# Optimization experiments

Measured on AMD Instinct MI355X. Metric: run time of the kernel, lower is better.

## Reference

```python
import jax, jax.numpy as jnp
import numpy as np

B, T, H = 2, 2048, 512
E, K, INTER = 8, 2, 1024


def setup_inputs() -> dict:
    key = jax.random.key(0)
    ks = jax.random.split(key, 8)
    s_h = 1.0 / np.sqrt(H)
    s_i = 1.0 / np.sqrt(INTER)
    return {
        "x": jax.random.normal(ks[0], (B, T, H), dtype=jnp.float32),
        "router_w": jax.random.normal(ks[1], (H, E), dtype=jnp.float32) * s_h,
        "Wg": jax.random.normal(ks[2], (E, H, INTER), dtype=jnp.float32) * s_h,
        "Wu": jax.random.normal(ks[3], (E, H, INTER), dtype=jnp.float32) * s_h,
        "Wd": jax.random.normal(ks[4], (E, INTER, H), dtype=jnp.float32) * s_i,
        "Sg": jax.random.normal(ks[5], (H, INTER), dtype=jnp.float32) * s_h,
        "Su": jax.random.normal(ks[6], (H, INTER), dtype=jnp.float32) * s_h,
        "Sd": jax.random.normal(ks[7], (INTER, H), dtype=jnp.float32) * s_i,
    }


def reference(x, router_w, Wg, Wu, Wd, Sg, Su, Sd):
    b, t, h = x.shape
    flat = x.reshape(b * t, h)                        # [N, H]
    n = flat.shape[0]

    # --- router: softmax over experts, top-k, renormalized top-k weights ---
    full_scores = jax.nn.softmax(flat @ router_w, axis=-1)   # [N, E]
    w, idx = jax.lax.top_k(full_scores, K)                   # [N, K]
    w = w / jnp.sum(w, axis=-1, keepdims=True)

    # dense combine-weight matrix: cw[n, e] = sum_j w[n, j] * (idx[n, j] == e)
    cw = jnp.zeros((n, E), dtype=flat.dtype).at[jnp.arange(n)[:, None], idx].add(w)

    # --- routed experts (SwiGLU), computed for all experts, combined by cw ---
    g = jnp.einsum("nh,ehi->eni", flat, Wg)          # [E, N, INTER]
    u = jnp.einsum("nh,ehi->eni", flat, Wu)
    y = jnp.einsum("eni,eih->enh", jax.nn.silu(g) * u, Wd)   # [E, N, H]
    out = jnp.einsum("ne,enh->nh", cw, y)            # [N, H]

    # --- shared expert(s) ---
    out = out + (jax.nn.silu(flat @ Sg) * (flat @ Su)) @ Sd

    return out.reshape(b, t, h)
```

## Files before the change

### kernel.cpp

```cpp
#include <hip/hip_runtime.h>

typedef unsigned short u16;
typedef u16 u16x8 __attribute__((ext_vector_type(8)));
typedef __bf16 bf16x8 __attribute__((ext_vector_type(8)));
typedef float f32x4 __attribute__((ext_vector_type(4)));

constexpr int NT   = 4096;
constexpr int HD   = 512;
constexpr int ID   = 1024;
constexpr int NEXP = 8;
constexpr int ROWCAP = 13312;
constexpr int MAXRB  = 104;

constexpr size_t OFF_XB   = 0;
constexpr size_t OFF_WGT  = OFF_XB   + (size_t)NT*HD*2;
constexpr size_t OFF_WUT  = OFF_WGT  + (size_t)NEXP*ID*HD*2;
constexpr size_t OFF_WDT  = OFF_WUT  + (size_t)NEXP*ID*HD*2;
constexpr size_t OFF_SGT  = OFF_WDT  + (size_t)NEXP*HD*ID*2;
constexpr size_t OFF_SUT  = OFF_SGT  + (size_t)ID*HD*2;
constexpr size_t OFF_SDT  = OFF_SUT  + (size_t)ID*HD*2;
constexpr size_t OFF_HBUF = OFF_SDT  + (size_t)HD*ID*2;
constexpr size_t OFF_TOK  = OFF_HBUF + (size_t)ROWCAP*ID*2;
constexpr size_t OFF_WGTW = OFF_TOK  + (size_t)ROWCAP*4;
constexpr size_t OFF_TI   = OFF_WGTW + (size_t)ROWCAP*4;
constexpr size_t OFF_TW   = OFF_TI   + (size_t)NT*16;
constexpr size_t OFF_META = OFF_TW   + (size_t)NT*8;
constexpr size_t WS_NEED  = OFF_META + 2048;

__device__ __forceinline__ u16 f2bf(float f){
  unsigned int u = __float_as_uint(f);
  u += 0x7fffu + ((u >> 16) & 1u);
  return (u16)(u >> 16);
}

#define AS1C(p) ((const __attribute__((address_space(1))) void*)(p))
#define AS3(p)  ((__attribute__((address_space(3))) void*)(p))
__device__ __forceinline__ void gld16(const void* g, void* l){
  __builtin_amdgcn_global_load_lds(AS1C(g), AS3(l), 16, 0, 0);
}

__global__ __launch_bounds__(256) void transpose_convert_kernel(
    const float* __restrict__ Wg, const float* __restrict__ Wu, const float* __restrict__ Wd,
    const float* __restrict__ Sg, const float* __restrict__ Su, const float* __restrict__ Sd,
    u16* __restrict__ WgT, u16* __restrict__ WuT, u16* __restrict__ WdT,
    u16* __restrict__ SgT, u16* __restrict__ SuT, u16* __restrict__ SdT)
{
  int b = blockIdx.x;
  const float* src; u16* dst; int R, C, t;
  if (b < 4096)      { int e=b>>9; t=b&511; src=Wg+(size_t)e*HD*ID; dst=WgT+(size_t)e*ID*HD; R=HD; C=ID; }
  else if (b < 8192) { b-=4096; int e=b>>9; t=b&511; src=Wu+(size_t)e*HD*ID; dst=WuT+(size_t)e*ID*HD; R=HD; C=ID; }
  else if (b < 12288){ b-=8192; int e=b>>9; t=b&511; src=Wd+(size_t)e*ID*HD; dst=WdT+(size_t)e*HD*ID; R=ID; C=HD; }
  else if (b < 12800){ t=b-12288; src=Sg; dst=SgT; R=HD; C=ID; }
  else if (b < 13312){ t=b-12800; src=Su; dst=SuT; R=HD; C=ID; }
  else               { t=b-13312; src=Sd; dst=SdT; R=ID; C=HD; }
  const int tc = C >> 5;
  const int r0 = (t / tc) << 5, c0 = (t % tc) << 5;
  __shared__ float tile[32][33];
  const int tx = threadIdx.x & 31, ty = threadIdx.x >> 5;
  #pragma unroll
  for (int j=0;j<4;j++) tile[ty+j*8][tx] = src[(size_t)(r0+ty+j*8)*C + c0+tx];
  __syncthreads();
  #pragma unroll
  for (int j=0;j<4;j++) dst[(size_t)(c0+ty+j*8)*R + r0+tx] = f2bf(tile[tx][ty+j*8]);
}

constexpr int RTOK = 32;
__global__ __launch_bounds__(256) void router_kernel(
    const float* __restrict__ x, const float* __restrict__ rw,
    u16* __restrict__ xb, int* __restrict__ tok, float* __restrict__ wgt,
    int4* __restrict__ tokinfo, float2* __restrict__ tw, int* __restrict__ cnt)
{
  const int wave = threadIdx.x >> 6, lane = threadIdx.x & 63;
  __shared__ int h[8];
  __shared__ int basev[8];
  __shared__ int s_e0[RTOK], s_e1[RTOK], s_l0[RTOK], s_l1[RTOK];
  __shared__ float s_w0[RTOK];
  if (threadIdx.x < 8) h[threadIdx.x] = 0;
  __syncthreads();

  #pragma unroll
  for (int t=0; t<RTOK/4; ++t){
    const int slot = wave*(RTOK/4) + t;
    const int n = blockIdx.x*RTOK + slot;
    const float4 xv0 = *(const float4*)(x + (size_t)n*HD + lane*8);
    const float4 xv1 = *(const float4*)(x + (size_t)n*HD + lane*8 + 4);
    u16x8 xs;
    xs[0]=f2bf(xv0.x); xs[1]=f2bf(xv0.y); xs[2]=f2bf(xv0.z); xs[3]=f2bf(xv0.w);
    xs[4]=f2bf(xv1.x); xs[5]=f2bf(xv1.y); xs[6]=f2bf(xv1.z); xs[7]=f2bf(xv1.w);
    *(u16x8*)(xb + (size_t)n*HD + lane*8) = xs;
    const float xa[8] = {xv0.x,xv0.y,xv0.z,xv0.w,xv1.x,xv1.y,xv1.z,xv1.w};
    float p[8] = {0,0,0,0,0,0,0,0};
    const float4* rp = (const float4*)(rw + (size_t)lane*8*NEXP);
    #pragma unroll
    for (int j=0;j<8;j++){
      float4 r0 = rp[j*2], r1 = rp[j*2+1];
      p[0]+=xa[j]*r0.x; p[1]+=xa[j]*r0.y; p[2]+=xa[j]*r0.z; p[3]+=xa[j]*r0.w;
      p[4]+=xa[j]*r1.x; p[5]+=xa[j]*r1.y; p[6]+=xa[j]*r1.z; p[7]+=xa[j]*r1.w;
    }
    #pragma unroll
    for (int m=1;m<64;m<<=1){
      #pragma unroll
      for (int e=0;e<8;e++) p[e] += __shfl_xor(p[e], m, 64);
    }
    if (lane == 0){
      int e0 = 0; float s0 = p[0];
      #pragma unroll
      for (int e=1;e<8;e++) if (p[e] > s0){ s0 = p[e]; e0 = e; }
      int e1 = -1; float s1 = -3.4e38f;
      #pragma unroll
      for (int e=0;e<8;e++) if (e != e0 && p[e] > s1){ s1 = p[e]; e1 = e; }
      s_e0[slot] = e0; s_e1[slot] = e1;
      s_w0[slot] = 1.f / (1.f + expf(s1 - s0));
      s_l0[slot] = atomicAdd(&h[e0], 1);
      s_l1[slot] = atomicAdd(&h[e1], 1);
    }
  }
  __syncthreads();
  if (threadIdx.x < 8)
    basev[threadIdx.x] = atomicAdd(cnt + threadIdx.x*16, h[threadIdx.x]);
  __syncthreads();
  if (threadIdx.x < RTOK){
    const int slot = threadIdx.x;
    const int n = blockIdx.x*RTOK + slot;
    const int e0 = s_e0[slot], e1 = s_e1[slot];
    const float w0 = s_w0[slot];
    tokinfo[n] = make_int4(e0, e1, basev[e0]+s_l0[slot], basev[e1]+s_l1[slot]);
    tw[n] = make_float2(w0, 1.f - w0);
    tok[n] = n;
    wgt[n] = 1.0f;
  }
}

__global__ __launch_bounds__(256) void build_lists_kernel(
    int* __restrict__ meta, int* __restrict__ tok, float* __restrict__ wgt,
    const int4* __restrict__ tokinfo, const float2* __restrict__ tw)
{
  __shared__ int s_off[9];
  const int t = threadIdx.x;
  if (t == 0){
    int off = NT;
    for (int e=0;e<NEXP;e++){ meta[200+e] = off; off += ((meta[e*16]+127)>>7)<<7; }
    meta[208] = off;
    meta[210] = off >> 7;
    for (int rb=0; rb<32; rb++) meta[212+rb] = 8;
    for (int e=0;e<NEXP;e++){
      int b0 = meta[200+e] >> 7, b1 = meta[201+e] >> 7;
      for (int rb=b0; rb<b1; rb++) meta[212+rb] = e;
    }
    for (int e=0;e<9;e++) s_off[e] = meta[200+e];
  }
  __syncthreads();
  const int end = s_off[8];
  for (int i = NT + t; i < end; i += 256) tok[i] = -1;
  __syncthreads();
  for (int n = t; n < NT; n += 256){
    int4 ti = tokinfo[n];
    float2 w = tw[n];
    int a0 = s_off[ti.x] + ti.z; tok[a0] = n; wgt[a0] = w.x;
    int a1 = s_off[ti.y] + ti.w; tok[a1] = n; wgt[a1] = w.y;
  }
}

__global__ __launch_bounds__(256,2) void gemm1_kernel(
    const u16* __restrict__ xb, const u16* __restrict__ WgT, const u16* __restrict__ WuT,
    const u16* __restrict__ SgT, const u16* __restrict__ SuT,
    const int* __restrict__ tok, const int* __restrict__ meta, u16* __restrict__ Hbuf)
{
  const int rb = blockIdx.y;
  if (rb >= meta[210]) return;
  const int e = meta[212+rb];
  const u16* __restrict__ Bg = (e < NEXP) ? (WgT + (size_t)e*ID*HD) : SgT;
  const u16* __restrict__ Bu = (e < NEXP) ? (WuT + (size_t)e*ID*HD) : SuT;
  const int n0 = blockIdx.x << 7;
  const int a0 = rb << 7;
  __shared__ u16 smem[24576];
  u16* sA = smem; u16* sG = smem + 8192; u16* sU = smem + 16384;
  const int tid = threadIdx.x;
  const int wave = tid >> 6, lane = tid & 63;
  const int wr = wave >> 1, wc = wave & 1;
  const int kb = (lane & 7) ^ (lane >> 3);
  const int sw = (lane & 7) << 3;
  int trowA[4];
  #pragma unroll
  for (int r=0;r<4;r++){
    int row = (wave*4+r)*8 + (lane>>3);
    int tt = tok[a0 + row];
    trowA[r] = (tt < 0) ? 0 : tt;
  }
  f32x4 accG[4][4], accU[4][4];
  const f32x4 zz = {0.f,0.f,0.f,0.f};
  #pragma unroll
  for (int mi=0;mi<4;mi++)
    #pragma unroll
    for (int ni=0;ni<4;ni++){ accG[mi][ni] = zz; accU[mi][ni] = zz; }

  for (int it=0; it<HD/64; ++it){
    const int k0 = it*64;
    #pragma unroll
    for (int r=0;r<4;r++){
      const int chunk = wave*4 + r;
      const int row = chunk*8 + (lane>>3);
      gld16(xb + (size_t)trowA[r]*HD + k0 + kb*8, sA + chunk*512);
      gld16(Bg + (size_t)(n0+row)*HD + k0 + kb*8, sG + chunk*512);
      gld16(Bu + (size_t)(n0+row)*HD + k0 + kb*8, sU + chunk*512);
    }
    __syncthreads();
    #pragma unroll
    for (int ks=0; ks<2; ++ks){
      const int ko = ks*32 + ((lane>>4)<<3);
      const int kx = ko ^ sw;
      bf16x8 av[4];
      #pragma unroll
      for (int mi=0;mi<4;mi++)
        av[mi] = *(const bf16x8*)(sA + (wr*64+mi*16+(lane&15))*64 + kx);
      #pragma unroll
      for (int ni=0;ni<4;ni++){
        bf16x8 gv = *(const bf16x8*)(sG + (wc*64+ni*16+(lane&15))*64 + kx);
        bf16x8 uv = *(const bf16x8*)(sU + (wc*64+ni*16+(lane&15))*64 + kx);
        #pragma unroll
        for (int mi=0;mi<4;mi++){
          accG[mi][ni] = __builtin_amdgcn_mfma_f32_16x16x32_bf16(av[mi], gv, accG[mi][ni], 0,0,0);
          accU[mi][ni] = __builtin_amdgcn_mfma_f32_16x16x32_bf16(av[mi], uv, accU[mi][ni], 0,0,0);
        }
      }
    }
    __syncthreads();
  }
  u16* hT = smem;
  #pragma unroll
  for (int mi=0;mi<4;mi++){
    #pragma unroll
    for (int ni=0;ni<4;ni++){
      const int col = wc*64 + ni*16 + (lane&15);
      #pragma unroll
      for (int j=0;j<4;j++){
        const int row = wr*64 + mi*16 + ((lane>>4)<<2) + j;
        const float g = accG[mi][ni][j], u = accU[mi][ni][j];
        const float h = (g / (1.f + __expf(-g))) * u;
        hT[row*128 + col] = f2bf(h);
      }
    }
  }
  __syncthreads();
  #pragma unroll
  for (int r=0;r<8;r++){
    const int o = r*2048 + tid*8;
    const int row = o >> 7, col = o & 127;
    *(u16x8*)(Hbuf + (size_t)(a0+row)*ID + n0 + col) = *(const u16x8*)(hT + o);
  }
}

__global__ __launch_bounds__(256,2) void gemm2_kernel(
    const u16* __restrict__ Hbuf, const u16* __restrict__ WdT, const u16* __restrict__ SdT,
    const int* __restrict__ tok, const float* __restrict__ wgt,
    const int* __restrict__ meta, float* __restrict__ out)
{
  const int rb = blockIdx.y;
  if (rb >= meta[210]) return;
  const int e = meta[212+rb];
  const u16* __restrict__ Bd = (e < NEXP) ? (WdT + (size_t)e*HD*ID) : SdT;
  const int n0 = blockIdx.x << 7;
  const int a0 = rb << 7;
  __shared__ u16 smem[16384];
  u16* sA = smem; u16* sB = smem + 8192;
  const int tid = threadIdx.x;
  const int wave = tid >> 6, lane = tid & 63;
  const int wr = wave >> 1, wc = wave & 1;
  const int kb = (lane & 7) ^ (lane >> 3);
  const int sw = (lane & 7) << 3;
  f32x4 acc[4][4];
  const f32x4 zz = {0.f,0.f,0.f,0.f};
  #pragma unroll
  for (int mi=0;mi<4;mi++)
    #pragma unroll
    for (int ni=0;ni<4;ni++) acc[mi][ni] = zz;

  for (int it=0; it<ID/64; ++it){
    const int k0 = it*64;
    #pragma unroll
    for (int r=0;r<4;r++){
      const int chunk = wave*4 + r;
      const int row = chunk*8 + (lane>>3);
      gld16(Hbuf + (size_t)(a0+row)*ID + k0 + kb*8, sA + chunk*512);
      gld16(Bd   + (size_t)(n0+row)*ID + k0 + kb*8, sB + chunk*512);
    }
    __syncthreads();
    #pragma unroll
    for (int ks=0; ks<2; ++ks){
      const int ko = ks*32 + ((lane>>4)<<3);
      const int kx = ko ^ sw;
      bf16x8 av[4];
      #pragma unroll
      for (int mi=0;mi<4;mi++)
        av[mi] = *(const bf16x8*)(sA + (wr*64+mi*16+(lane&15))*64 + kx);
      #pragma unroll
      for (int ni=0;ni<4;ni++){
        bf16x8 bv = *(const bf16x8*)(sB + (wc*64+ni*16+(lane&15))*64 + kx);
        #pragma unroll
        for (int mi=0;mi<4;mi++)
          acc[mi][ni] = __builtin_amdgcn_mfma_f32_16x16x32_bf16(av[mi], bv, acc[mi][ni], 0,0,0);
      }
    }
    __syncthreads();
  }
  #pragma unroll
  for (int mi=0;mi<4;mi++){
    #pragma unroll
    for (int j=0;j<4;j++){
      const int row = wr*64 + mi*16 + ((lane>>4)<<2) + j;
      const int a = a0 + row;
      const int t = tok[a];
      if (t < 0) continue;
      const float w = wgt[a];
      float* orow = out + (size_t)t*HD + n0 + wc*64 + (lane&15);
      #pragma unroll
      for (int ni=0;ni<4;ni++)
        atomicAdd(orow + ni*16, w * acc[mi][ni][j]);
    }
  }
}

extern "C" void kernel_launch(void* const* d_in, const int* in_sizes, int n_in,
                              void* d_out, int out_size, void* d_ws, size_t ws_size,
                              hipStream_t stream)
{
  (void)in_sizes; (void)n_in;
  if (ws_size < WS_NEED) return;
  const float* x  = (const float*)d_in[0];
  const float* rw = (const float*)d_in[1];
  const float* Wg = (const float*)d_in[2];
  const float* Wu = (const float*)d_in[3];
  const float* Wd = (const float*)d_in[4];
  const float* Sg = (const float*)d_in[5];
  const float* Su = (const float*)d_in[6];
  const float* Sd = (const float*)d_in[7];
  float* out = (float*)d_out;
  char* ws = (char*)d_ws;
  u16*   xb   = (u16*)  (ws + OFF_XB);
  u16*   WgT  = (u16*)  (ws + OFF_WGT);
  u16*   WuT  = (u16*)  (ws + OFF_WUT);
  u16*   WdT  = (u16*)  (ws + OFF_WDT);
  u16*   SgT  = (u16*)  (ws + OFF_SGT);
  u16*   SuT  = (u16*)  (ws + OFF_SUT);
  u16*   SdT  = (u16*)  (ws + OFF_SDT);
  u16*   Hbuf = (u16*)  (ws + OFF_HBUF);
  int*   tok  = (int*)  (ws + OFF_TOK);
  float* wgt  = (float*)(ws + OFF_WGTW);
  int4*  ti   = (int4*) (ws + OFF_TI);
  float2* tw  = (float2*)(ws + OFF_TW);
  int*   meta = (int*)  (ws + OFF_META);

  hipMemsetAsync(out, 0, (size_t)out_size * sizeof(float), stream);
  hipMemsetAsync(meta, 0, 512, stream);

  transpose_convert_kernel<<<13824, 256, 0, stream>>>(Wg,Wu,Wd,Sg,Su,Sd, WgT,WuT,WdT,SgT,SuT,SdT);
  router_kernel<<<NT/RTOK, 256, 0, stream>>>(x, rw, xb, tok, wgt, ti, tw, meta);
  build_lists_kernel<<<1, 256, 0, stream>>>(meta, tok, wgt, ti, tw);
  gemm1_kernel<<<dim3(ID/128, MAXRB), 256, 0, stream>>>(xb, WgT, WuT, SgT, SuT, tok, meta, Hbuf);
  gemm2_kernel<<<dim3(HD/128, MAXRB), 256, 0, stream>>>(Hbuf, WdT, SdT, tok, wgt, meta, out);
}
```

Before: 231.4 us.

## Replace gemm2 atomic scatter with bf16 staging buffer and gather combine kernel

gemm2 no longer performs weighted atomicAdd into the fp32 output. It writes unweighted per-row results in bf16 to a staging buffer that reuses the WgT/WuT workspace region. A new combine kernel gathers each token's shared-expert row and its two routed rows, applies the routing weights, and writes the output directly, so the output memset is no longer needed. This removes atomic contention and the memset at the cost of an extra launch, an extra bf16 round-trip (precision loss on expert outputs), and reliance on the shared-expert rows being laid out at row index n.

```diff
diff --git a/kernel.cpp b/kernel.cpp
--- a/kernel.cpp
+++ b/kernel.cpp
@@ -26,11 +26,16 @@
 constexpr size_t OFF_TW   = OFF_TI   + (size_t)NT*16;
 constexpr size_t OFF_META = OFF_TW   + (size_t)NT*8;
 constexpr size_t WS_NEED  = OFF_META + 2048;
+constexpr size_t OFF_YB   = OFF_WGT;
+static_assert((size_t)ROWCAP*HD*2 <= (size_t)2*NEXP*ID*HD*2, "Ybuf must fit in WgT+WuT");
 
 __device__ __forceinline__ u16 f2bf(float f){
   unsigned int u = __float_as_uint(f);
   u += 0x7fffu + ((u >> 16) & 1u);
   return (u16)(u >> 16);
+}
+__device__ __forceinline__ float bf2f(u16 v){
+  return __uint_as_float(((unsigned int)v) << 16);
 }
 
 #define AS1C(p) ((const __attribute__((address_space(1))) void*)(p))
@@ -252,8 +257,7 @@
 
 __global__ __launch_bounds__(256,2) void gemm2_kernel(
     const u16* __restrict__ Hbuf, const u16* __restrict__ WdT, const u16* __restrict__ SdT,
-    const int* __restrict__ tok, const float* __restrict__ wgt,
-    const int* __restrict__ meta, float* __restrict__ out)
+    const int* __restrict__ tok, const int* __restrict__ meta, u16* __restrict__ Ybuf)
 {
   const int rb = blockIdx.y;
   if (rb >= meta[210]) return;
@@ -309,22 +313,47 @@
     for (int j=0;j<4;j++){
       const int row = wr*64 + mi*16 + ((lane>>4)<<2) + j;
       const int a = a0 + row;
-      const int t = tok[a];
-      if (t < 0) continue;
-      const float w = wgt[a];
-      float* orow = out + (size_t)t*HD + n0 + wc*64 + (lane&15);
+      if (tok[a] < 0) continue;
+      u16* yrow = Ybuf + (size_t)a*HD + n0 + wc*64 + (lane&15);
       #pragma unroll
       for (int ni=0;ni<4;ni++)
-        atomicAdd(orow + ni*16, w * acc[mi][ni][j]);
-    }
-  }
+        yrow[ni*16] = f2bf(acc[mi][ni][j]);
+    }
+  }
+}
+
+__global__ __launch_bounds__(256) void combine_kernel(
+    const u16* __restrict__ Ybuf, const int4* __restrict__ tokinfo,
+    const float2* __restrict__ tw, const int* __restrict__ meta,
+    float* __restrict__ out)
+{
+  const int wave = threadIdx.x >> 6, lane = threadIdx.x & 63;
+  const int n = blockIdx.x*4 + wave;
+  const int4 ti = tokinfo[n];
+  const float2 w = tw[n];
+  const int r0 = meta[200+ti.x] + ti.z;
+  const int r1 = meta[200+ti.y] + ti.w;
+  const size_t c = (size_t)lane*8;
+  const u16x8 ys = *(const u16x8*)(Ybuf + (size_t)n*HD + c);
+  const u16x8 y0 = *(const u16x8*)(Ybuf + (size_t)r0*HD + c);
+  const u16x8 y1 = *(const u16x8*)(Ybuf + (size_t)r1*HD + c);
+  float4 o0, o1;
+  float* o = (float*)&o0;
+  #pragma unroll
+  for (int j=0;j<8;j++){
+    float r = bf2f(ys[j]) + w.x*bf2f(y0[j]) + w.y*bf2f(y1[j]);
+    if (j < 4) ((float*)&o0)[j] = r; else ((float*)&o1)[j-4] = r;
+  }
+  (void)o;
+  float4* op = (float4*)(out + (size_t)n*HD + c);
+  op[0] = o0; op[1] = o1;
 }
 
 extern "C" void kernel_launch(void* const* d_in, const int* in_sizes, int n_in,
                               void* d_out, int out_size, void* d_ws, size_t ws_size,
                               hipStream_t stream)
 {
-  (void)in_sizes; (void)n_in;
+  (void)in_sizes; (void)n_in; (void)out_size;
   if (ws_size < WS_NEED) return;
   const float* x  = (const float*)d_in[0];
   const float* rw = (const float*)d_in[1];
@@ -344,18 +373,19 @@
   u16*   SuT  = (u16*)  (ws + OFF_SUT);
   u16*   SdT  = (u16*)  (ws + OFF_SDT);
   u16*   Hbuf = (u16*)  (ws + OFF_HBUF);
+  u16*   Ybuf = (u16*)  (ws + OFF_YB);
   int*   tok  = (int*)  (ws + OFF_TOK);
   float* wgt  = (float*)(ws + OFF_WGTW);
   int4*  ti   = (int4*) (ws + OFF_TI);
   float2* tw  = (float2*)(ws + OFF_TW);
   int*   meta = (int*)  (ws + OFF_META);
 
-  hipMemsetAsync(out, 0, (size_t)out_size * sizeof(float), stream);
   hipMemsetAsync(meta, 0, 512, stream);
 
   transpose_convert_kernel<<<13824, 256, 0, stream>>>(Wg,Wu,Wd,Sg,Su,Sd, WgT,WuT,WdT,SgT,SuT,SdT);
   router_kernel<<<NT/RTOK, 256, 0, stream>>>(x, rw, xb, tok, wgt, ti, tw, meta);
   build_lists_kernel<<<1, 256, 0, stream>>>(meta, tok, wgt, ti, tw);
   gemm1_kernel<<<dim3(ID/128, MAXRB), 256, 0, stream>>>(xb, WgT, WuT, SgT, SuT, tok, meta, Hbuf);
-  gemm2_kernel<<<dim3(HD/128, MAXRB), 256, 0, stream>>>(Hbuf, WdT, SdT, tok, wgt, meta, out);
-}
+  gemm2_kernel<<<dim3(HD/128, MAXRB), 256, 0, stream>>>(Hbuf, WdT, SdT, tok, meta, Ybuf);
+  combine_kernel<<<NT/4, 256, 0, stream>>>(Ybuf, ti, tw, meta, out);
+}
```

Measured after the change: 220.5 us. 1.05x faster.
